# Performance work log

Measured on AMD Instinct MI355X. Metric: run time of the kernel, lower is better.

Reference implementation:

```python
import jax, jax.numpy as jnp
import numpy as np

EPS = 1e-8
BETA = 0.05
K = 8192
D = 256
M = 32768


def _l2_normalize(x, axis=-1):
    # matches torch F.normalize: x / max(||x||, eps)
    n = jnp.linalg.norm(x, axis=axis, keepdims=True)
    return x / jnp.maximum(n, EPS)


def setup_inputs() -> dict:
    key = jax.random.key(0)
    kz, ke = jax.random.split(key)
    z = jax.random.normal(kz, (M, D), dtype=jnp.float32)
    # codebook initialized as unit-norm rows, as in the torch __init__
    E = _l2_normalize(jax.random.normal(ke, (K, D), dtype=jnp.float32), axis=1)
    return {"z": z, "E": E}


def reference(z, E):
    z_flat = z.reshape(-1, z.shape[-1])          # [M, D]
    z_n = _l2_normalize(z_flat, axis=1)          # [M, D]
    E_n = _l2_normalize(E, axis=1)               # [K, D]
    sims = jnp.einsum('md,kd->mk', z_n, E_n)     # [M, K] cosine similarity
    idx = jnp.argmax(sims, axis=1)               # [M]
    zq = E[idx]                                  # [M, D] gather
    zq_n = _l2_normalize(zq, axis=1)
    commit = jnp.mean((jax.lax.stop_gradient(zq_n) - z_n) ** 2)
    codebk = jnp.mean((zq_n - jax.lax.stop_gradient(z_n)) ** 2)
    loss = commit + BETA * codebk
    zq_st = z_flat + jax.lax.stop_gradient(zq - z_flat)  # straight-through
    return loss, zq_st, idx
```

## Files before the change

### kernel.cpp

```cpp
#include <hip/hip_runtime.h>
#include <float.h>
#include <math.h>
#include <stdint.h>

#define M_ROWS 32768
#define K_CODES 8192
#define DDIM 256
#define BM 128
#define BN 64
#define NTILES (K_CODES / BN)
#define DELTA 0.009f
#define CAP 16

typedef __attribute__((ext_vector_type(8))) short short8;
typedef __attribute__((ext_vector_type(4))) float f32x4;

__device__ inline unsigned short f2bf(float f) {
    unsigned u = __float_as_uint(f);
    return (unsigned short)((u + 0x7fffu + ((u >> 16) & 1u)) >> 16);
}
__device__ inline unsigned fkey(float f) {
    unsigned u = __float_as_uint(f);
    return u ^ ((unsigned)((int)u >> 31) | 0x80000000u);
}
__device__ inline float fkey_inv(unsigned k) {
    unsigned u = (k & 0x80000000u) ? (k ^ 0x80000000u) : ~k;
    return __uint_as_float(u);
}

#define GLOAD16(gsrc, ldst)                                                     \
    __builtin_amdgcn_global_load_lds(                                           \
        (const __attribute__((address_space(1))) void*)(gsrc),                  \
        (__attribute__((address_space(3))) void*)(ldst), 16, 0, 0)

__global__ __launch_bounds__(256) void k_norm_E(const float* __restrict__ E,
                                                float* __restrict__ En,
                                                unsigned short* __restrict__ En_b) {
    int wid  = threadIdx.x >> 6;
    int lane = threadIdx.x & 63;
    int row  = blockIdx.x * 4 + wid;
    const float* e = E + (size_t)row * DDIM;
    float v[4];
    float ssq = 0.f;
#pragma unroll
    for (int p = 0; p < 4; ++p) { v[p] = e[lane + 64 * p]; ssq += v[p] * v[p]; }
#pragma unroll
    for (int off = 32; off >= 1; off >>= 1) ssq += __shfl_xor(ssq, off);
    float inv = 1.f / fmaxf(sqrtf(ssq), 1e-8f);
    float* o = En + (size_t)row * DDIM;
    unsigned short* ob = En_b + (size_t)row * DDIM;
#pragma unroll
    for (int p = 0; p < 4; ++p) {
        float nv = v[p] * inv;
        o[lane + 64 * p]  = nv;
        ob[lane + 64 * p] = f2bf(nv);
    }
}

__global__ __launch_bounds__(512, 2) void k_cand(
    const float* __restrict__ z,
    const unsigned short* __restrict__ En_b,
    unsigned char* __restrict__ cand_cnt,
    int* __restrict__ cand_k) {

    __shared__ __attribute__((aligned(16))) char Bw[8][2][8192];
    __shared__ unsigned rowmaxKey[BM];
    __shared__ int cnt[BM];
    __shared__ int list[BM][CAP];

    const int tid  = threadIdx.x;
    const int lane = tid & 63;
    const int wid  = tid >> 6;
    const int wr   = wid >> 2;
    const int wc   = wid & 3;
    const int lo   = lane & 15;
    const int hi   = lane >> 4;
    const int m0   = blockIdx.x * BM;

    if (tid < BM) { cnt[tid] = 0; rowmaxKey[tid] = 0u; }

    const char* eb = (const char*)En_b;
    char* b0 = &Bw[wid][0][0];
    char* b1 = &Bw[wid][1][0];

    auto stage = [&](int ktile, char* bufp) {
#pragma unroll
        for (int i = 0; i < 8; ++i) {
            int G   = i * 64 + lane;
            int row = G >> 5;
            int g   = (G & 31) ^ (row & 7);
            GLOAD16(eb + (size_t)(ktile * BN + wc * 16 + row) * 512 + g * 16,
                    bufp + i * 1024);
        }
    };

    stage(0, b0);
    stage(1, b1);
    __syncthreads();

    short8 af[4][8];
#pragma unroll
    for (int mi = 0; mi < 4; ++mi) {
        const float* zr = z + (size_t)(m0 + wr * 64 + mi * 16 + lo) * DDIM;
        float4 v[16];
        float ssq = 0.f;
#pragma unroll
        for (int ks = 0; ks < 8; ++ks) {
            int e0 = (ks * 4 + hi) * 8;
            v[2 * ks]     = *(const float4*)&zr[e0];
            v[2 * ks + 1] = *(const float4*)&zr[e0 + 4];
            float4 a = v[2 * ks], b = v[2 * ks + 1];
            ssq += a.x * a.x + a.y * a.y + a.z * a.z + a.w * a.w;
            ssq += b.x * b.x + b.y * b.y + b.z * b.z + b.w * b.w;
        }
        ssq += __shfl_xor(ssq, 16);
        ssq += __shfl_xor(ssq, 32);
        float inv = 1.f / fmaxf(sqrtf(ssq), 1e-8f);
#pragma unroll
        for (int ks = 0; ks < 8; ++ks) {
            float4 a = v[2 * ks], b = v[2 * ks + 1];
            short8 s8;
            s8[0] = (short)f2bf(a.x * inv); s8[1] = (short)f2bf(a.y * inv);
            s8[2] = (short)f2bf(a.z * inv); s8[3] = (short)f2bf(a.w * inv);
            s8[4] = (short)f2bf(b.x * inv); s8[5] = (short)f2bf(b.y * inv);
            s8[6] = (short)f2bf(b.z * inv); s8[7] = (short)f2bf(b.w * inv);
            af[mi][ks] = s8;
        }
    }

    float pmax[16];
#pragma unroll
    for (int s = 0; s < 16; ++s) pmax[s] = -FLT_MAX;

    for (int t = 0; t < NTILES; ++t) {
        if (t < NTILES - 1) asm volatile("s_waitcnt vmcnt(8)" ::: "memory");
        else                asm volatile("s_waitcnt vmcnt(0)" ::: "memory");
        __builtin_amdgcn_sched_barrier(0);

        const unsigned short* Bc = (const unsigned short*)((t & 1) ? b1 : b0);
        f32x4 acc[4];
#pragma unroll
        for (int mi = 0; mi < 4; ++mi) acc[mi] = (f32x4){0.f, 0.f, 0.f, 0.f};
#pragma unroll
        for (int ks = 0; ks < 8; ++ks) {
            int g = (ks * 4 + hi) ^ (lo & 7);
            short8 bf = *(const short8*)&Bc[lo * 256 + g * 8];
#pragma unroll
            for (int mi = 0; mi < 4; ++mi)
                acc[mi] = __builtin_amdgcn_mfma_f32_16x16x32_bf16(af[mi][ks], bf, acc[mi], 0, 0, 0);
        }
#pragma unroll
        for (int mi = 0; mi < 4; ++mi)
#pragma unroll
            for (int r = 0; r < 4; ++r)
                pmax[mi * 4 + r] = fmaxf(pmax[mi * 4 + r], acc[mi][r]);

        if (t + 2 < NTILES) stage(t + 2, (t & 1) ? b1 : b0);
    }

#pragma unroll
    for (int s = 0; s < 16; ++s) {
        float w = pmax[s];
        w = fmaxf(w, __shfl_xor(w, 1));
        w = fmaxf(w, __shfl_xor(w, 2));
        w = fmaxf(w, __shfl_xor(w, 4));
        w = fmaxf(w, __shfl_xor(w, 8));
        if (lo == 0) {
            int row = wr * 64 + (s >> 2) * 16 + hi * 4 + (s & 3);
            atomicMax(&rowmaxKey[row], fkey(w));
        }
    }
    __syncthreads();

    float thr[16];
#pragma unroll
    for (int s = 0; s < 16; ++s) {
        int row = wr * 64 + (s >> 2) * 16 + hi * 4 + (s & 3);
        thr[s] = fkey_inv(rowmaxKey[row]) - DELTA;
    }

    stage(0, b0);
    stage(1, b1);

    for (int t = 0; t < NTILES; ++t) {
        if (t < NTILES - 1) asm volatile("s_waitcnt vmcnt(8)" ::: "memory");
        else                asm volatile("s_waitcnt vmcnt(0)" ::: "memory");
        __builtin_amdgcn_sched_barrier(0);

        const unsigned short* Bc = (const unsigned short*)((t & 1) ? b1 : b0);
        f32x4 acc[4];
#pragma unroll
        for (int mi = 0; mi < 4; ++mi) acc[mi] = (f32x4){0.f, 0.f, 0.f, 0.f};
#pragma unroll
        for (int ks = 0; ks < 8; ++ks) {
            int g = (ks * 4 + hi) ^ (lo & 7);
            short8 bf = *(const short8*)&Bc[lo * 256 + g * 8];
#pragma unroll
            for (int mi = 0; mi < 4; ++mi)
                acc[mi] = __builtin_amdgcn_mfma_f32_16x16x32_bf16(af[mi][ks], bf, acc[mi], 0, 0, 0);
        }

        const int kv = t * BN + wc * 16 + lo;
#pragma unroll
        for (int mi = 0; mi < 4; ++mi)
#pragma unroll
            for (int r = 0; r < 4; ++r) {
                if (acc[mi][r] >= thr[mi * 4 + r]) {
                    int row = wr * 64 + mi * 16 + hi * 4 + r;
                    int pos = atomicAdd(&cnt[row], 1);
                    if (pos < CAP) list[row][pos] = kv;
                }
            }

        if (t + 2 < NTILES) stage(t + 2, (t & 1) ? b1 : b0);
    }
    __syncthreads();

    if (tid < BM) {
        int c = cnt[tid];
        cand_cnt[m0 + tid] = (unsigned char)(c > CAP ? 255 : c);
        int n = c < CAP ? c : CAP;
        for (int j = 0; j < n; ++j) cand_k[(size_t)(m0 + tid) * CAP + j] = list[tid][j];
    }
}

__global__ __launch_bounds__(256) void k_final(const float* __restrict__ z,
                                               const float* __restrict__ E,
                                               const float* __restrict__ En,
                                               const unsigned char* __restrict__ cand_cnt,
                                               const int* __restrict__ cand_k,
                                               float* __restrict__ out,
                                               float* __restrict__ rowloss) {
    __shared__ float zl[4][256];
    int wid  = threadIdx.x >> 6;
    int lane = threadIdx.x & 63;
    int m    = blockIdx.x * 4 + wid;

    const float* zr = z + (size_t)m * DDIM;
    const float4 zz = *(const float4*)&zr[lane * 4];

    int   c  = cand_cnt[m];
    float bv = -FLT_MAX;
    int   bk = 0x7fffffff;
    if (c != 255) {
        for (int j = 0; j < c; ++j) {
            int k = cand_k[(size_t)m * CAP + j];
            const float4 ee = *(const float4*)&En[(size_t)k * DDIM + lane * 4];
            float s = zz.x * ee.x + zz.y * ee.y + zz.z * ee.z + zz.w * ee.w;
#pragma unroll
            for (int off = 1; off < 64; off <<= 1) s += __shfl_xor(s, off);
            if (s > bv || (s == bv && k < bk)) { bv = s; bk = k; }
        }
    } else {
        *(float4*)&zl[wid][lane * 4] = zz;
        asm volatile("s_waitcnt lgkmcnt(0)" ::: "memory");
        for (int kb = 0; kb < K_CODES; kb += 64) {
            int k = kb + lane;
            const float4* er = (const float4*)&En[(size_t)k * DDIM];
            float s0 = 0.f, s1 = 0.f, s2 = 0.f, s3 = 0.f;
#pragma unroll 8
            for (int d4 = 0; d4 < 64; ++d4) {
                float4 e  = er[d4];
                float4 zd = *(const float4*)&zl[wid][d4 * 4];
                s0 += zd.x * e.x; s1 += zd.y * e.y;
                s2 += zd.z * e.z; s3 += zd.w * e.w;
            }
            float s = (s0 + s1) + (s2 + s3);
            if (s > bv || (s == bv && k < bk)) { bv = s; bk = k; }
        }
#pragma unroll
        for (int off = 1; off < 64; off <<= 1) {
            float ov = __shfl_xor(bv, off);
            int   ok = __shfl_xor(bk, off);
            if (ov > bv || (ov == bv && ok < bk)) { bv = ov; bk = ok; }
        }
    }
    const int idx = bk;

    const float* er = E + (size_t)idx * DDIM;
    float zv[4], ev[4];
    float sz = 0.f, se = 0.f;
#pragma unroll
    for (int p = 0; p < 4; ++p) {
        zv[p] = zr[lane + 64 * p]; sz += zv[p] * zv[p];
        ev[p] = er[lane + 64 * p]; se += ev[p] * ev[p];
    }
#pragma unroll
    for (int off = 32; off >= 1; off >>= 1) {
        sz += __shfl_xor(sz, off);
        se += __shfl_xor(se, off);
    }
    float nz = fmaxf(sqrtf(sz), 1e-8f);
    float ne = fmaxf(sqrtf(se), 1e-8f);

    float rs = 0.f;
    float* zq = out + 1 + (size_t)m * DDIM;
#pragma unroll
    for (int p = 0; p < 4; ++p) {
        float zn = zv[p] / nz;
        float en = ev[p] / ne;
        float d  = en - zn;
        rs += d * d;
        zq[lane + 64 * p] = zv[p] + (ev[p] - zv[p]);
    }
#pragma unroll
    for (int off = 32; off >= 1; off >>= 1) rs += __shfl_xor(rs, off);

    if (lane == 0) {
        rowloss[m] = rs;
        out[1 + (size_t)M_ROWS * DDIM + m] = (float)idx;
    }
}

__global__ __launch_bounds__(256) void k_loss(const float* __restrict__ rowloss,
                                              float* __restrict__ out) {
    __shared__ double sm[256];
    double s = 0.0;
    for (int i = threadIdx.x; i < M_ROWS; i += 256) s += (double)rowloss[i];
    sm[threadIdx.x] = s;
    __syncthreads();
    for (int st = 128; st > 0; st >>= 1) {
        if (threadIdx.x < st) sm[threadIdx.x] += sm[threadIdx.x + st];
        __syncthreads();
    }
    if (threadIdx.x == 0) {
        float c = (float)(sm[0] / (double)((size_t)M_ROWS * DDIM));
        out[0] = c + 0.05f * c;
    }
}

extern "C" void kernel_launch(void* const* d_in, const int* in_sizes, int n_in,
                              void* d_out, int out_size, void* d_ws, size_t ws_size,
                              hipStream_t stream) {
    const float* z = (const float*)d_in[0];
    const float* E = (const float*)d_in[1];
    float* out = (float*)d_out;

    char* ws = (char*)d_ws;
    size_t off = 0;
    float*          En       = (float*)(ws + off);          off += (size_t)K_CODES * DDIM * 4;
    unsigned short* En_b     = (unsigned short*)(ws + off); off += (size_t)K_CODES * DDIM * 2;
    int*            cand_k   = (int*)(ws + off);            off += (size_t)M_ROWS * CAP * 4;
    unsigned char*  cand_cnt = (unsigned char*)(ws + off);  off += (size_t)M_ROWS;
    float*          rowloss  = (float*)(ws + off);

    k_norm_E<<<K_CODES / 4, 256, 0, stream>>>(E, En, En_b);
    k_cand<<<M_ROWS / BM, 512, 0, stream>>>(z, En_b, cand_cnt, cand_k);
    k_final<<<M_ROWS / 4, 256, 0, stream>>>(z, E, En, cand_cnt, cand_k, out, rowloss);
    k_loss<<<1, 256, 0, stream>>>(rowloss, out);
}
```

Measured before the change: 353.1 us.

## Load codebook fragments directly into registers and reshape block tile to 64x128

```diff
diff --git a/kernel.cpp b/kernel.cpp
--- a/kernel.cpp
+++ b/kernel.cpp
@@ -6,8 +6,8 @@
 #define M_ROWS 32768
 #define K_CODES 8192
 #define DDIM 256
-#define BM 128
-#define BN 64
+#define BM 64
+#define BN 128
 #define NTILES (K_CODES / BN)
 #define DELTA 0.009f
 #define CAP 16
@@ -27,11 +27,6 @@
     unsigned u = (k & 0x80000000u) ? (k ^ 0x80000000u) : ~k;
     return __uint_as_float(u);
 }
-
-#define GLOAD16(gsrc, ldst)                                                     \
-    __builtin_amdgcn_global_load_lds(                                           \
-        (const __attribute__((address_space(1))) void*)(gsrc),                  \
-        (__attribute__((address_space(3))) void*)(ldst), 16, 0, 0)
 
 __global__ __launch_bounds__(256) void k_norm_E(const float* __restrict__ E,
                                                 float* __restrict__ En,
@@ -63,7 +58,6 @@
     unsigned char* __restrict__ cand_cnt,
     int* __restrict__ cand_k) {
 
-    __shared__ __attribute__((aligned(16))) char Bw[8][2][8192];
     __shared__ unsigned rowmaxKey[BM];
     __shared__ int cnt[BM];
     __shared__ int list[BM][CAP];
@@ -71,37 +65,30 @@
     const int tid  = threadIdx.x;
     const int lane = tid & 63;
     const int wid  = tid >> 6;
-    const int wr   = wid >> 2;
-    const int wc   = wid & 3;
     const int lo   = lane & 15;
     const int hi   = lane >> 4;
     const int m0   = blockIdx.x * BM;
 
     if (tid < BM) { cnt[tid] = 0; rowmaxKey[tid] = 0u; }
-
-    const char* eb = (const char*)En_b;
-    char* b0 = &Bw[wid][0][0];
-    char* b1 = &Bw[wid][1][0];
-
-    auto stage = [&](int ktile, char* bufp) {
-#pragma unroll
-        for (int i = 0; i < 8; ++i) {
-            int G   = i * 64 + lane;
-            int row = G >> 5;
-            int g   = (G & 31) ^ (row & 7);
-            GLOAD16(eb + (size_t)(ktile * BN + wc * 16 + row) * 512 + g * 16,
-                    bufp + i * 1024);
-        }
-    };
-
-    stage(0, b0);
-    stage(1, b1);
     __syncthreads();
 
+    const char* bbase = (const char*)En_b + (size_t)(wid * 16 + lo) * 512 + hi * 16;
+
+#define LOADT(buf, t)                                                           \
+    {                                                                           \
+        const char* bp_ = bbase + (size_t)(t) * (BN * 512);                     \
+        _Pragma("unroll")                                                       \
+        for (int ks_ = 0; ks_ < 8; ++ks_)                                       \
+            buf[ks_] = *(const short8*)(bp_ + ks_ * 64);                        \
+    }
+
+    short8 bA[8], bB[8];
+    LOADT(bA, 0);
+
     short8 af[4][8];
 #pragma unroll
     for (int mi = 0; mi < 4; ++mi) {
-        const float* zr = z + (size_t)(m0 + wr * 64 + mi * 16 + lo) * DDIM;
+        const float* zr = z + (size_t)(m0 + mi * 16 + lo) * DDIM;
         float4 v[16];
         float ssq = 0.f;
 #pragma unroll
@@ -128,34 +115,35 @@
         }
     }
 
+#define MFMA_TILE(buf, acc)                                                     \
+    _Pragma("unroll")                                                           \
+    for (int ks_ = 0; ks_ < 8; ++ks_) {                                         \
+        _Pragma("unroll")                                                       \
+        for (int mi_ = 0; mi_ < 4; ++mi_)                                       \
+            acc[mi_] = __builtin_amdgcn_mfma_f32_16x16x32_bf16(                 \
+                af[mi_][ks_], buf[ks_], acc[mi_], 0, 0, 0);                     \
+    }
+
     float pmax[16];
 #pragma unroll
     for (int s = 0; s < 16; ++s) pmax[s] = -FLT_MAX;
 
-    for (int t = 0; t < NTILES; ++t) {
-        if (t < NTILES - 1) asm volatile("s_waitcnt vmcnt(8)" ::: "memory");
-        else                asm volatile("s_waitcnt vmcnt(0)" ::: "memory");
-        __builtin_amdgcn_sched_barrier(0);
-
-        const unsigned short* Bc = (const unsigned short*)((t & 1) ? b1 : b0);
-        f32x4 acc[4];
-#pragma unroll
-        for (int mi = 0; mi < 4; ++mi) acc[mi] = (f32x4){0.f, 0.f, 0.f, 0.f};
-#pragma unroll
-        for (int ks = 0; ks < 8; ++ks) {
-            int g = (ks * 4 + hi) ^ (lo & 7);
-            short8 bf = *(const short8*)&Bc[lo * 256 + g * 8];
-#pragma unroll
-            for (int mi = 0; mi < 4; ++mi)
-                acc[mi] = __builtin_amdgcn_mfma_f32_16x16x32_bf16(af[mi][ks], bf, acc[mi], 0, 0, 0);
-        }
-#pragma unroll
-        for (int mi = 0; mi < 4; ++mi)
-#pragma unroll
-            for (int r = 0; r < 4; ++r)
-                pmax[mi * 4 + r] = fmaxf(pmax[mi * 4 + r], acc[mi][r]);
-
-        if (t + 2 < NTILES) stage(t + 2, (t & 1) ? b1 : b0);
+#define COMPA(buf)                                                              \
+    {                                                                           \
+        f32x4 acc[4];                                                           \
+        _Pragma("unroll") for (int mi_ = 0; mi_ < 4; ++mi_)                     \
+            acc[mi_] = (f32x4){0.f, 0.f, 0.f, 0.f};                             \
+        MFMA_TILE(buf, acc)                                                     \
+        _Pragma("unroll") for (int mi_ = 0; mi_ < 4; ++mi_)                     \
+            _Pragma("unroll") for (int r_ = 0; r_ < 4; ++r_)                    \
+                pmax[mi_ * 4 + r_] = fmaxf(pmax[mi_ * 4 + r_], acc[mi_][r_]);   \
+    }
+
+    for (int t = 0; t < NTILES; t += 2) {
+        LOADT(bB, t + 1);
+        COMPA(bA);
+        if (t + 2 < NTILES) LOADT(bA, t + 2);
+        COMPA(bB);
     }
 
 #pragma unroll
@@ -166,7 +154,7 @@
         w = fmaxf(w, __shfl_xor(w, 4));
         w = fmaxf(w, __shfl_xor(w, 8));
         if (lo == 0) {
-            int row = wr * 64 + (s >> 2) * 16 + hi * 4 + (s & 3);
+            int row = (s >> 2) * 16 + hi * 4 + (s & 3);
             atomicMax(&rowmaxKey[row], fkey(w));
         }
     }
@@ -175,44 +163,33 @@
     float thr[16];
 #pragma unroll
     for (int s = 0; s < 16; ++s) {
-        int row = wr * 64 + (s >> 2) * 16 + hi * 4 + (s & 3);
+        int row = (s >> 2) * 16 + hi * 4 + (s & 3);
         thr[s] = fkey_inv(rowmaxKey[row]) - DELTA;
     }
 
-    stage(0, b0);
-    stage(1, b1);
-
-    for (int t = 0; t < NTILES; ++t) {
-        if (t < NTILES - 1) asm volatile("s_waitcnt vmcnt(8)" ::: "memory");
-        else                asm volatile("s_waitcnt vmcnt(0)" ::: "memory");
-        __builtin_amdgcn_sched_barrier(0);
-
-        const unsigned short* Bc = (const unsigned short*)((t & 1) ? b1 : b0);
-        f32x4 acc[4];
-#pragma unroll
-        for (int mi = 0; mi < 4; ++mi) acc[mi] = (f32x4){0.f, 0.f, 0.f, 0.f};
-#pragma unroll
-        for (int ks = 0; ks < 8; ++ks) {
-            int g = (ks * 4 + hi) ^ (lo & 7);
-            short8 bf = *(const short8*)&Bc[lo * 256 + g * 8];
-#pragma unroll
-            for (int mi = 0; mi < 4; ++mi)
-                acc[mi] = __builtin_amdgcn_mfma_f32_16x16x32_bf16(af[mi][ks], bf, acc[mi], 0, 0, 0);
-        }
-
-        const int kv = t * BN + wc * 16 + lo;
-#pragma unroll
-        for (int mi = 0; mi < 4; ++mi)
-#pragma unroll
-            for (int r = 0; r < 4; ++r) {
-                if (acc[mi][r] >= thr[mi * 4 + r]) {
-                    int row = wr * 64 + mi * 16 + hi * 4 + r;
-                    int pos = atomicAdd(&cnt[row], 1);
-                    if (pos < CAP) list[row][pos] = kv;
-                }
-            }
-
-        if (t + 2 < NTILES) stage(t + 2, (t & 1) ? b1 : b0);
+#define COMPB(buf, t)                                                           \
+    {                                                                           \
+        f32x4 acc[4];                                                           \
+        _Pragma("unroll") for (int mi_ = 0; mi_ < 4; ++mi_)                     \
+            acc[mi_] = (f32x4){0.f, 0.f, 0.f, 0.f};                             \
+        MFMA_TILE(buf, acc)                                                     \
+        const int kv_ = (t) * BN + wid * 16 + lo;                               \
+        _Pragma("unroll") for (int mi_ = 0; mi_ < 4; ++mi_)                     \
+            _Pragma("unroll") for (int r_ = 0; r_ < 4; ++r_) {                  \
+                if (acc[mi_][r_] >= thr[mi_ * 4 + r_]) {                        \
+                    int row_ = mi_ * 16 + hi * 4 + r_;                          \
+                    int pos_ = atomicAdd(&cnt[row_], 1);                        \
+                    if (pos_ < CAP) list[row_][pos_] = kv_;                     \
+                }                                                               \
+            }                                                                   \
+    }
+
+    LOADT(bA, 0);
+    for (int t = 0; t < NTILES; t += 2) {
+        LOADT(bB, t + 1);
+        COMPB(bA, t);
+        if (t + 2 < NTILES) LOADT(bA, t + 2);
+        COMPB(bB, t + 1);
     }
     __syncthreads();
 
@@ -222,6 +199,10 @@
         int n = c < CAP ? c : CAP;
         for (int j = 0; j < n; ++j) cand_k[(size_t)(m0 + tid) * CAP + j] = list[tid][j];
     }
+#undef LOADT
+#undef MFMA_TILE
+#undef COMPA
+#undef COMPB
 }
 
 __global__ __launch_bounds__(256) void k_final(const float* __restrict__ z,
```

New measurement: 574.9 us. 62.8% more time.

## Replace two-pass candidate search with single-pass top-2 tracking and column rescans

Applied to the files above, without the earlier changes.

```diff
diff --git a/kernel.cpp b/kernel.cpp
--- a/kernel.cpp
+++ b/kernel.cpp
@@ -6,11 +6,12 @@
 #define M_ROWS 32768
 #define K_CODES 8192
 #define DDIM 256
-#define BM 128
+#define BM 64
 #define BN 64
 #define NTILES (K_CODES / BN)
 #define DELTA 0.009f
 #define CAP 16
+#define FLAGBIT 0x10000
 
 typedef __attribute__((ext_vector_type(8))) short short8;
 typedef __attribute__((ext_vector_type(4))) float f32x4;
@@ -57,13 +58,13 @@
     }
 }
 
-__global__ __launch_bounds__(512, 2) void k_cand(
+__global__ __launch_bounds__(256, 1) void k_cand(
     const float* __restrict__ z,
     const unsigned short* __restrict__ En_b,
     unsigned char* __restrict__ cand_cnt,
     int* __restrict__ cand_k) {
 
-    __shared__ __attribute__((aligned(16))) char Bw[8][2][8192];
+    __shared__ __attribute__((aligned(16))) char Bs[2][32768];
     __shared__ unsigned rowmaxKey[BM];
     __shared__ int cnt[BM];
     __shared__ int list[BM][CAP];
@@ -71,8 +72,6 @@
     const int tid  = threadIdx.x;
     const int lane = tid & 63;
     const int wid  = tid >> 6;
-    const int wr   = wid >> 2;
-    const int wc   = wid & 3;
     const int lo   = lane & 15;
     const int hi   = lane >> 4;
     const int m0   = blockIdx.x * BM;
@@ -80,28 +79,24 @@
     if (tid < BM) { cnt[tid] = 0; rowmaxKey[tid] = 0u; }
 
     const char* eb = (const char*)En_b;
-    char* b0 = &Bw[wid][0][0];
-    char* b1 = &Bw[wid][1][0];
 
     auto stage = [&](int ktile, char* bufp) {
 #pragma unroll
         for (int i = 0; i < 8; ++i) {
-            int G   = i * 64 + lane;
+            int chunk = i * 4 + wid;
+            int G   = chunk * 64 + lane;
             int row = G >> 5;
             int g   = (G & 31) ^ (row & 7);
-            GLOAD16(eb + (size_t)(ktile * BN + wc * 16 + row) * 512 + g * 16,
-                    bufp + i * 1024);
+            GLOAD16(eb + (size_t)(ktile * BN + row) * 512 + g * 16, bufp + chunk * 1024);
         }
     };
 
-    stage(0, b0);
-    stage(1, b1);
-    __syncthreads();
+    stage(0, &Bs[0][0]);
 
     short8 af[4][8];
 #pragma unroll
     for (int mi = 0; mi < 4; ++mi) {
-        const float* zr = z + (size_t)(m0 + wr * 64 + mi * 16 + lo) * DDIM;
+        const float* zr = z + (size_t)(m0 + mi * 16 + lo) * DDIM;
         float4 v[16];
         float ssq = 0.f;
 #pragma unroll
@@ -128,91 +123,72 @@
         }
     }
 
-    float pmax[16];
-#pragma unroll
-    for (int s = 0; s < 16; ++s) pmax[s] = -FLT_MAX;
+    float v1[16], v2[16];
+    int   k1[16];
+#pragma unroll
+    for (int s = 0; s < 16; ++s) { v1[s] = -FLT_MAX; v2[s] = -FLT_MAX; k1[s] = 0; }
+
+    __syncthreads();
+
+    const int brow = wid * 16 + lo;
+    const int bsw  = brow & 7;
 
     for (int t = 0; t < NTILES; ++t) {
-        if (t < NTILES - 1) asm volatile("s_waitcnt vmcnt(8)" ::: "memory");
-        else                asm volatile("s_waitcnt vmcnt(0)" ::: "memory");
-        __builtin_amdgcn_sched_barrier(0);
-
-        const unsigned short* Bc = (const unsigned short*)((t & 1) ? b1 : b0);
+        if (t + 1 < NTILES) stage(t + 1, &Bs[(t + 1) & 1][0]);
+
         f32x4 acc[4];
 #pragma unroll
         for (int mi = 0; mi < 4; ++mi) acc[mi] = (f32x4){0.f, 0.f, 0.f, 0.f};
+        const unsigned short* Bc = (const unsigned short*)&Bs[t & 1][0];
 #pragma unroll
         for (int ks = 0; ks < 8; ++ks) {
-            int g = (ks * 4 + hi) ^ (lo & 7);
-            short8 bf = *(const short8*)&Bc[lo * 256 + g * 8];
+            short8 bf = *(const short8*)&Bc[brow * 256 + (((ks * 4 + hi) ^ bsw)) * 8];
 #pragma unroll
             for (int mi = 0; mi < 4; ++mi)
                 acc[mi] = __builtin_amdgcn_mfma_f32_16x16x32_bf16(af[mi][ks], bf, acc[mi], 0, 0, 0);
         }
+
+        const int kv = t * BN + wid * 16 + lo;
 #pragma unroll
         for (int mi = 0; mi < 4; ++mi)
 #pragma unroll
-            for (int r = 0; r < 4; ++r)
-                pmax[mi * 4 + r] = fmaxf(pmax[mi * 4 + r], acc[mi][r]);
-
-        if (t + 2 < NTILES) stage(t + 2, (t & 1) ? b1 : b0);
+            for (int r = 0; r < 4; ++r) {
+                int s = mi * 4 + r;
+                float v = acc[mi][r];
+                v2[s] = fmaxf(v2[s], fminf(v1[s], v));
+                k1[s] = (v > v1[s]) ? kv : k1[s];
+                v1[s] = fmaxf(v1[s], v);
+            }
+
+        __syncthreads();
     }
 
 #pragma unroll
     for (int s = 0; s < 16; ++s) {
-        float w = pmax[s];
+        float w = v1[s];
         w = fmaxf(w, __shfl_xor(w, 1));
         w = fmaxf(w, __shfl_xor(w, 2));
         w = fmaxf(w, __shfl_xor(w, 4));
         w = fmaxf(w, __shfl_xor(w, 8));
         if (lo == 0) {
-            int row = wr * 64 + (s >> 2) * 16 + hi * 4 + (s & 3);
+            int row = (s >> 2) * 16 + hi * 4 + (s & 3);
             atomicMax(&rowmaxKey[row], fkey(w));
         }
     }
     __syncthreads();
 
-    float thr[16];
 #pragma unroll
     for (int s = 0; s < 16; ++s) {
-        int row = wr * 64 + (s >> 2) * 16 + hi * 4 + (s & 3);
-        thr[s] = fkey_inv(rowmaxKey[row]) - DELTA;
-    }
-
-    stage(0, b0);
-    stage(1, b1);
-
-    for (int t = 0; t < NTILES; ++t) {
-        if (t < NTILES - 1) asm volatile("s_waitcnt vmcnt(8)" ::: "memory");
-        else                asm volatile("s_waitcnt vmcnt(0)" ::: "memory");
-        __builtin_amdgcn_sched_barrier(0);
-
-        const unsigned short* Bc = (const unsigned short*)((t & 1) ? b1 : b0);
-        f32x4 acc[4];
-#pragma unroll
-        for (int mi = 0; mi < 4; ++mi) acc[mi] = (f32x4){0.f, 0.f, 0.f, 0.f};
-#pragma unroll
-        for (int ks = 0; ks < 8; ++ks) {
-            int g = (ks * 4 + hi) ^ (lo & 7);
-            short8 bf = *(const short8*)&Bc[lo * 256 + g * 8];
-#pragma unroll
-            for (int mi = 0; mi < 4; ++mi)
-                acc[mi] = __builtin_amdgcn_mfma_f32_16x16x32_bf16(af[mi][ks], bf, acc[mi], 0, 0, 0);
-        }
-
-        const int kv = t * BN + wc * 16 + lo;
-#pragma unroll
-        for (int mi = 0; mi < 4; ++mi)
-#pragma unroll
-            for (int r = 0; r < 4; ++r) {
-                if (acc[mi][r] >= thr[mi * 4 + r]) {
-                    int row = wr * 64 + mi * 16 + hi * 4 + r;
-                    int pos = atomicAdd(&cnt[row], 1);
-                    if (pos < CAP) list[row][pos] = kv;
-                }
-            }
-
-        if (t + 2 < NTILES) stage(t + 2, (t & 1) ? b1 : b0);
+        int row = (s >> 2) * 16 + hi * 4 + (s & 3);
+        float thr = fkey_inv(rowmaxKey[row]) - DELTA;
+        if (v1[s] >= thr) {
+            int pos = atomicAdd(&cnt[row], 1);
+            if (pos < CAP) list[row][pos] = k1[s];
+        }
+        if (v2[s] >= thr) {
+            int pos = atomicAdd(&cnt[row], 1);
+            if (pos < CAP) list[row][pos] = FLAGBIT | (wid * 16 + lo);
+        }
     }
     __syncthreads();
 
@@ -224,13 +200,15 @@
     }
 }
 
-__global__ __launch_bounds__(256) void k_final(const float* __restrict__ z,
-                                               const float* __restrict__ E,
-                                               const float* __restrict__ En,
-                                               const unsigned char* __restrict__ cand_cnt,
-                                               const int* __restrict__ cand_k,
-                                               float* __restrict__ out,
-                                               float* __restrict__ rowloss) {
+__global__ __launch_bounds__(256, 1) void k_final(
+    const float* __restrict__ z,
+    const float* __restrict__ E,
+    const float* __restrict__ En,
+    const unsigned char* __restrict__ cand_cnt,
+    const int* __restrict__ cand_k,
+    float* __restrict__ out,
+    float* __restrict__ rowloss) {
+
     __shared__ float zl[4][256];
     int wid  = threadIdx.x >> 6;
     int lane = threadIdx.x & 63;
@@ -238,27 +216,19 @@
 
     const float* zr = z + (size_t)m * DDIM;
     const float4 zz = *(const float4*)&zr[lane * 4];
-
-    int   c  = cand_cnt[m];
+    *(float4*)&zl[wid][lane * 4] = zz;
+    asm volatile("s_waitcnt lgkmcnt(0)" ::: "memory");
+
     float bv = -FLT_MAX;
     int   bk = 0x7fffffff;
-    if (c != 255) {
-        for (int j = 0; j < c; ++j) {
-            int k = cand_k[(size_t)m * CAP + j];
-            const float4 ee = *(const float4*)&En[(size_t)k * DDIM + lane * 4];
-            float s = zz.x * ee.x + zz.y * ee.y + zz.z * ee.z + zz.w * ee.w;
-#pragma unroll
-            for (int off = 1; off < 64; off <<= 1) s += __shfl_xor(s, off);
-            if (s > bv || (s == bv && k < bk)) { bv = s; bk = k; }
-        }
-    } else {
-        *(float4*)&zl[wid][lane * 4] = zz;
-        asm volatile("s_waitcnt lgkmcnt(0)" ::: "memory");
-        for (int kb = 0; kb < K_CODES; kb += 64) {
-            int k = kb + lane;
+
+    auto rescan = [&](int cb) {
+#pragma unroll
+        for (int j = 0; j < 2; ++j) {
+            int k = cb + (lane * 2 + j) * 64;
             const float4* er = (const float4*)&En[(size_t)k * DDIM];
             float s0 = 0.f, s1 = 0.f, s2 = 0.f, s3 = 0.f;
-#pragma unroll 8
+#pragma unroll 16
             for (int d4 = 0; d4 < 64; ++d4) {
                 float4 e  = er[d4];
                 float4 zd = *(const float4*)&zl[wid][d4 * 4];
@@ -268,12 +238,30 @@
             float s = (s0 + s1) + (s2 + s3);
             if (s > bv || (s == bv && k < bk)) { bv = s; bk = k; }
         }
-#pragma unroll
-        for (int off = 1; off < 64; off <<= 1) {
-            float ov = __shfl_xor(bv, off);
-            int   ok = __shfl_xor(bk, off);
-            if (ov > bv || (ov == bv && ok < bk)) { bv = ov; bk = ok; }
-        }
+    };
+
+    int c = cand_cnt[m];
+    if (c != 255) {
+        for (int j = 0; j < c; ++j) {
+            int e = cand_k[(size_t)m * CAP + j];
+            if (e < FLAGBIT) {
+                const float4 ee = *(const float4*)&En[(size_t)e * DDIM + lane * 4];
+                float s = zz.x * ee.x + zz.y * ee.y + zz.z * ee.z + zz.w * ee.w;
+#pragma unroll
+                for (int off = 1; off < 64; off <<= 1) s += __shfl_xor(s, off);
+                if (s > bv || (s == bv && e < bk)) { bv = s; bk = e; }
+            } else {
+                rescan(e & 63);
+            }
+        }
+    } else {
+        for (int cb = 0; cb < 64; ++cb) rescan(cb);
+    }
+#pragma unroll
+    for (int off = 1; off < 64; off <<= 1) {
+        float ov = __shfl_xor(bv, off);
+        int   ok = __shfl_xor(bk, off);
+        if (ov > bv || (ov == bv && ok < bk)) { bv = ov; bk = ok; }
     }
     const int idx = bk;
 
@@ -345,7 +333,7 @@
     float*          rowloss  = (float*)(ws + off);
 
     k_norm_E<<<K_CODES / 4, 256, 0, stream>>>(E, En, En_b);
-    k_cand<<<M_ROWS / BM, 512, 0, stream>>>(z, En_b, cand_cnt, cand_k);
+    k_cand<<<M_ROWS / BM, 256, 0, stream>>>(z, En_b, cand_cnt, cand_k);
     k_final<<<M_ROWS / 4, 256, 0, stream>>>(z, E, En, cand_cnt, cand_k, out, rowloss);
     k_loss<<<1, 256, 0, stream>>>(rowloss, out);
 }
```

After: 427.0 us. +20.9%, slower.
